# Optimization experiments

Measured on AMD Instinct MI355X. Metric: run time of the kernel, lower is better.

The kernel has to match this reference:

```python
import jax, jax.numpy as jnp
import numpy as np

D_MODEL = 1024
N_HEADS = 16
D_HEAD = D_MODEL // N_HEADS


def setup_inputs() -> dict:
    key = jax.random.key(0)
    ks = jax.random.split(key, 11)
    B, S = 2, 2048
    scale = 1.0 / np.sqrt(D_MODEL)
    inp = {
        "query": jax.random.normal(ks[0], (B, S, D_MODEL), jnp.float32),
        "key": jax.random.normal(ks[1], (B, S, D_MODEL), jnp.float32),
        "value": jax.random.normal(ks[2], (B, S, D_MODEL), jnp.float32),
        "Wq": jax.random.normal(ks[3], (D_MODEL, D_MODEL), jnp.float32) * scale,
        "bq": jnp.zeros((D_MODEL,), jnp.float32),
        "Wk": jax.random.normal(ks[4], (D_MODEL, D_MODEL), jnp.float32) * scale,
        "bk": jnp.zeros((D_MODEL,), jnp.float32),
        "Wv": jax.random.normal(ks[5], (D_MODEL, D_MODEL), jnp.float32) * scale,
        "bv": jnp.zeros((D_MODEL,), jnp.float32),
        "Wo": jax.random.normal(ks[6], (D_MODEL, D_MODEL), jnp.float32) * scale,
        "bo": jnp.zeros((D_MODEL,), jnp.float32),
    }
    return inp


def _split_heads(x):
    B, S, _ = x.shape
    return x.reshape(B, S, N_HEADS, D_HEAD).transpose(0, 2, 1, 3)  # [B,H,S,Dh]


def reference(query, key, value, Wq, bq, Wk, bk, Wv, bv, Wo, bo):
    q = _split_heads(query @ Wq + bq)
    k = _split_heads(key @ Wk + bk)
    v = _split_heads(value @ Wv + bv)
    # scores [B,H,S,S] -- faithfully materialized as in the original
    scores = jnp.einsum("bhqd,bhkd->bhqk", q, k) / np.sqrt(D_HEAD)
    attn = jax.nn.softmax(scores, axis=-1)
    out = jnp.einsum("bhqk,bhkd->bhqd", attn, v)  # [B,H,S,Dh]
    B, H, S, Dh = out.shape
    out = out.transpose(0, 2, 1, 3).reshape(B, S, H * Dh)
    return out @ Wo + bo
```

## Files before the change

kernel.cpp:

```cpp
#include <hip/hip_runtime.h>
#include <hip/hip_bf16.h>

using bf16 = __hip_bfloat16;
typedef __bf16 bf16x8 __attribute__((ext_vector_type(8)));
typedef __bf16 bf16x2v __attribute__((ext_vector_type(2)));
typedef float f32x4 __attribute__((ext_vector_type(4)));
typedef float f32x16 __attribute__((ext_vector_type(16)));

#define SEQ 2048
#define DM  1024
#define QSCALE 0.18033688011112042f

__device__ __forceinline__ f32x4 mfma16(bf16x8 a, bf16x8 b, f32x4 c) {
  return __builtin_amdgcn_mfma_f32_16x16x32_bf16(a, b, c, 0, 0, 0);
}
__device__ __forceinline__ f32x16 mfma32(bf16x8 a, bf16x8 b, f32x16 c) {
  return __builtin_amdgcn_mfma_f32_32x32x16_bf16(a, b, c, 0, 0, 0);
}
__device__ __forceinline__ void gload16(const void* g, void* l) {
  __builtin_amdgcn_global_load_lds(
      (const __attribute__((address_space(1))) unsigned int*)g,
      (__attribute__((address_space(3))) unsigned int*)l, 16, 0, 0);
}
__device__ __forceinline__ unsigned short bfbits(float x) {
  bf16 h = __float2bfloat16(x);
  return *reinterpret_cast<unsigned short*>(&h);
}
__device__ __forceinline__ unsigned pk2(float a, float b) {
#if __has_builtin(__builtin_amdgcn_cvt_pk_bf16_f32)
  bf16x2v r = __builtin_amdgcn_cvt_pk_bf16_f32(a, b);
  return *reinterpret_cast<unsigned*>(&r);
#else
  return (unsigned)bfbits(a) | ((unsigned)bfbits(b) << 16);
#endif
}
__device__ __forceinline__ float fexp2(float x) {
#if __has_builtin(__builtin_amdgcn_exp2f)
  return __builtin_amdgcn_exp2f(x);
#else
  return exp2f(x);
#endif
}
__device__ __forceinline__ void plswap(unsigned& a, unsigned& b) {
  asm("v_permlane32_swap_b32 %0, %1" : "+v"(a), "+v"(b));
}

__global__ __launch_bounds__(256) void cast_all(const float* __restrict__ q,
                                                const float* __restrict__ k,
                                                const float* __restrict__ v,
                                                const float* __restrict__ Wq,
                                                const float* __restrict__ Wk,
                                                const float* __restrict__ Wv,
                                                const float* __restrict__ Wo,
                                                bf16* __restrict__ Lx,
                                                bf16* __restrict__ Lw,
                                                bf16* __restrict__ Lwo) {
  __shared__ float tf[64][68];
  if (blockIdx.y < 3) {
    const float* src = blockIdx.y == 0 ? q : (blockIdx.y == 1 ? k : v);
    bf16* dst = Lx + (size_t)blockIdx.y * (4096ull * 1024) + (size_t)blockIdx.x * 16384;
#pragma unroll
    for (int i = 0; i < 8; ++i) {
      int u = threadIdx.x + i * 256;
      int k32 = u >> 6, l = u & 63;
      const float* p = src + (size_t)(blockIdx.x * 16 + (l & 15)) * 1024 + k32 * 32 + (l >> 4) * 8;
      float4 a = *(const float4*)p;
      float4 b = *(const float4*)(p + 4);
      alignas(16) unsigned o[4] = {pk2(a.x, a.y), pk2(a.z, a.w), pk2(b.x, b.y), pk2(b.z, b.w)};
      *(uint4*)(dst + (size_t)u * 8) = *(const uint4*)o;
    }
    return;
  }
  const int widx = blockIdx.y - 3;
  const float* W = widx == 0 ? Wq : (widx == 1 ? Wk : (widx == 2 ? Wv : Wo));
  bf16* dst = widx < 3 ? (Lw + (size_t)widx * 1048576) : Lwo;
  const int t = threadIdx.x, bx = blockIdx.x & 15, by = blockIdx.x >> 4;
#pragma unroll
  for (int i = 0; i < 4; ++i) {
    int u = t + i * 256, r = u >> 4, c4 = u & 15;
    *(float4*)&tf[r][c4 * 4] = *(const float4*)(W + (size_t)(by * 64 + r) * 1024 + bx * 64 + c4 * 4);
  }
  __syncthreads();
#pragma unroll
  for (int i = 0; i < 2; ++i) {
    int u = t + i * 256;
    int sub = u >> 6, l = u & 63;
    int n16l = sub >> 1, k32l = sub & 1;
    int nn = n16l * 16 + (l & 15);
    int kk = k32l * 32 + (l >> 4) * 8;
    alignas(16) unsigned o[4];
#pragma unroll
    for (int p = 0; p < 4; ++p) o[p] = pk2(tf[kk + 2 * p][nn], tf[kk + 2 * p + 1][nn]);
    size_t off = ((((size_t)(bx * 4 + n16l)) * 32 + (by * 2 + k32l)) * 64 + l) * 8;
    *(uint4*)(dst + off) = *(const uint4*)o;
  }
}

__global__ __launch_bounds__(512, 4) void qkv_gemm(const bf16* __restrict__ Lw,
                                                   const bf16* __restrict__ Lx,
                                                   const float* __restrict__ bq,
                                                   const float* __restrict__ bk,
                                                   const float* __restrict__ bv,
                                                   bf16* __restrict__ Lq,
                                                   bf16* __restrict__ Lk,
                                                   bf16* __restrict__ Lv) {
  __shared__ alignas(16) bf16 At[2][8192];
  __shared__ alignas(16) bf16 Bt[2][4096];
  const int t = threadIdx.x, lane = t & 63, w = t >> 6;
  const int m16 = lane & 15, g4 = lane >> 4;
  const int bid = blockIdx.x;
  const int logical = (bid & 7) * 48 + (bid >> 3);
  const int third = logical >> 7;
  const int r = logical & 127;
  const int shift = third < 2 ? 5 : 3;
  const int mt = r >> shift, nt = r & ((1 << shift) - 1);
  const int wm = w >> 1, wn = w & 1;
  const bf16* Wb = Lw + (size_t)third * 1048576;
  const bf16* Xb = Lx + (size_t)third * (4096ull * 1024);
  const bf16* Asrc = third < 2 ? Wb : Xb;
  const bf16* Bsrc = third < 2 ? Xb : Wb;
  f32x4 acc[4][4] = {};

#pragma unroll
  for (int ii = 0; ii < 3; ++ii) {
    int u = w * 3 + ii;
    if (u < 16)
      gload16(Asrc + (((size_t)(mt * 16 + u) * 32 + 0) * 64 + lane) * 8, (void*)&At[0][u * 512]);
    else
      gload16(Bsrc + (((size_t)(nt * 8 + u - 16) * 32 + 0) * 64 + lane) * 8, (void*)&Bt[0][(u - 16) * 512]);
  }

  int cur = 0;
  for (int k = 0; k < 32; ++k) {
    __builtin_amdgcn_s_barrier();
    __builtin_amdgcn_sched_barrier(0);
    if (k < 31) {
      const int nb = cur ^ 1;
#pragma unroll
      for (int ii = 0; ii < 3; ++ii) {
        int u = w * 3 + ii;
        if (u < 16)
          gload16(Asrc + (((size_t)(mt * 16 + u) * 32 + k + 1) * 64 + lane) * 8, (void*)&At[nb][u * 512]);
        else
          gload16(Bsrc + (((size_t)(nt * 8 + u - 16) * 32 + k + 1) * 64 + lane) * 8,
                  (void*)&Bt[nb][(u - 16) * 512]);
      }
      asm volatile("s_waitcnt vmcnt(3)" ::: "memory");
    } else {
      asm volatile("s_waitcnt vmcnt(0)" ::: "memory");
    }
    __builtin_amdgcn_sched_barrier(0);
    __builtin_amdgcn_s_barrier();
    __builtin_amdgcn_sched_barrier(0);

    bf16x8 afr[4], bfr[4];
#pragma unroll
    for (int i = 0; i < 4; ++i) afr[i] = *(const bf16x8*)&At[cur][(wm * 4 + i) * 512 + lane * 8];
#pragma unroll
    for (int j = 0; j < 4; ++j) bfr[j] = *(const bf16x8*)&Bt[cur][(wn * 4 + j) * 512 + lane * 8];
    __builtin_amdgcn_s_setprio(1);
#pragma unroll
    for (int i = 0; i < 4; ++i)
#pragma unroll
      for (int j = 0; j < 4; ++j) acc[i][j] = mfma16(afr[i], bfr[j], acc[i][j]);
    __builtin_amdgcn_s_setprio(0);
    cur ^= 1;
  }

  if (third < 2) {
    bf16* dst = third == 0 ? Lq : Lk;
    const float* bias = third == 0 ? bq : bk;
    const float sc = third == 0 ? QSCALE : 1.0f;
#pragma unroll
    for (int mi = 0; mi < 4; ++mi) {
      int doutb = mt * 256 + wm * 64 + mi * 16 + g4 * 4;
      float4 b4 = *(const float4*)(bias + doutb);
      int hh = doutb >> 6, d32 = (doutb & 63) >> 5;
      int lhi = (doutb & 31) >> 3, half = g4 & 1;
#pragma unroll
      for (int nj = 0; nj < 4; ++nj) {
        int seq = nt * 128 + wn * 64 + nj * 16 + m16;
        int bb2 = seq >> 11, s16w = (seq & 2047) >> 4;
        size_t off = ((((size_t)(bb2 * 128 + s16w)) * 16 + hh) * 2 + d32) * 512 + (m16 + 16 * lhi) * 8 + half * 4;
        uint2 pv;
        pv.x = pk2((acc[mi][nj][0] + b4.x) * sc, (acc[mi][nj][1] + b4.y) * sc);
        pv.y = pk2((acc[mi][nj][2] + b4.z) * sc, (acc[mi][nj][3] + b4.w) * sc);
        *(uint2*)(dst + off) = pv;
      }
    }
  } else {
#pragma unroll
    for (int nj = 0; nj < 4; ++nj) {
      int dout = nt * 128 + wn * 64 + nj * 16 + m16;
      float bvv = bv[dout];
      int hh = dout >> 6, dt = (dout & 63) >> 4;
#pragma unroll
      for (int mi = 0; mi < 4; ++mi) {
        int seqb = mt * 256 + wm * 64 + mi * 16 + g4 * 4;
        int b_ = seqb >> 11, kt = (seqb & 2047) >> 6, ks32 = (seqb & 63) >> 5;
        int lhi = (seqb & 31) >> 3, half = g4 & 1;
        size_t off = (((((size_t)(b_ * 32 + kt)) * 16 + hh) * 4 + dt) * 2 + ks32) * 512 + (m16 + 16 * lhi) * 8 + half * 4;
        uint2 pv;
        pv.x = pk2(acc[mi][nj][0] + bvv, acc[mi][nj][1] + bvv);
        pv.y = pk2(acc[mi][nj][2] + bvv, acc[mi][nj][3] + bvv);
        *(uint2*)(Lv + off) = pv;
      }
    }
  }
}

__global__ __launch_bounds__(512, 4) void flash(const bf16* __restrict__ Lq,
                                                const bf16* __restrict__ Lk,
                                                const bf16* __restrict__ Lv,
                                                bf16* __restrict__ Lab) {
  __shared__ alignas(16) unsigned char smem[65536];
  bf16* const Kb = (bf16*)smem;
  bf16* const Vb = (bf16*)(smem + 32768);

  const int t = threadIdx.x, lane = t & 63, w = t >> 6;
  const int l31 = lane & 31, m16 = lane & 15, hi = lane >> 5, b4 = (lane >> 4) & 1;
  const int qw = w >> 1, g = w & 1, wg = w >> 1;
  const int bid = blockIdx.x;
  const int logical = ((bid & 7) << 6) | (bid >> 3);
  const int qt = logical & 15, h = (logical >> 4) & 15, b = logical >> 8;

  bf16x8 qf[4];
  {
    const int sQ = b * 128 + qt * 8 + qw * 2 + b4;
#pragma unroll
    for (int ks = 0; ks < 4; ++ks) {
      const int d32 = ks >> 1, g4q = (ks & 1) * 2 + hi;
      qf[ks] = *(const bf16x8*)(Lq + (((size_t)sQ * 16 + h) * 2 + d32) * 512 + (m16 + 16 * g4q) * 8);
    }
  }

  const int ss = wg >> 1, sd = wg & 1;
#pragma unroll
  for (int u = 0; u < 2; ++u) {
    const bf16* gk = Lk + ((((size_t)(b * 128 + g * 64 + u * 2 + ss)) * 16 + h) * 2 + sd) * 512 + lane * 8;
    gload16(gk, (void*)(Kb + (g * 2 + 0) * 4096 + u * 2048 + wg * 512));
    const bf16* gv = Lv + (((((size_t)(b * 32 + g * 16)) * 16 + h) * 4 + wg) * 2 + u) * 512 + lane * 8;
    gload16(gv, (void*)(Vb + (g * 2 + 0) * 4096 + u * 2048 + wg * 512));
  }

  float lrow = 0.f;
  f32x16 oacc[2] = {};
  __syncthreads();

  for (int it = 0; it < 16; ++it) {
    const int cur = it & 1;
    const bf16* const Klb = Kb + (g * 2 + cur) * 4096;
    const bf16* const Vlb = Vb + (g * 2 + cur) * 4096;
    if (it < 15) {
      const int nb = cur ^ 1;
#pragma unroll
      for (int u = 0; u < 2; ++u) {
        const int kc = (it + 1) * 2 + u;
        const bf16* gk = Lk + ((((size_t)(b * 128 + g * 64 + kc * 2 + ss)) * 16 + h) * 2 + sd) * 512 + lane * 8;
        gload16(gk, (void*)(Kb + (g * 2 + nb) * 4096 + u * 2048 + wg * 512));
        const bf16* gv = Lv + (((((size_t)(b * 32 + g * 16 + (kc >> 1))) * 16 + h) * 4 + wg) * 2 + (kc & 1)) * 512 + lane * 8;
        gload16(gv, (void*)(Vb + (g * 2 + nb) * 4096 + u * 2048 + wg * 512));
      }
    }

#pragma unroll
    for (int u = 0; u < 2; ++u) {
      const bf16* const Kl = Klb + u * 2048;
      const bf16* const Vl = Vlb + u * 2048;

      f32x16 s = {};
      __builtin_amdgcn_s_setprio(1);
#pragma unroll
      for (int ks = 0; ks < 4; ++ks) {
        const int d32 = ks >> 1, g4k = (ks & 1) * 2 + hi;
        bf16x8 kf = *(const bf16x8*)&Kl[((b4 * 2 + d32) * 64 + m16 + 16 * g4k) * 8];
        s = mfma32(kf, qf[ks], s);
      }
      __builtin_amdgcn_s_setprio(0);

      float e[16];
#pragma unroll
      for (int r = 0; r < 16; ++r) e[r] = fexp2(s[r]);
      {
        float a0 = e[0] + e[1], a1 = e[2] + e[3], a2 = e[4] + e[5], a3 = e[6] + e[7];
        float a4 = e[8] + e[9], a5 = e[10] + e[11], a6 = e[12] + e[13], a7 = e[14] + e[15];
        lrow += ((a0 + a1) + (a2 + a3)) + ((a4 + a5) + (a6 + a7));
      }
      bf16x8 bP[2];
#pragma unroll
      for (int c = 0; c < 2; ++c) {
        unsigned P0 = pk2(e[8 * c + 0], e[8 * c + 1]);
        unsigned P1 = pk2(e[8 * c + 2], e[8 * c + 3]);
        unsigned P2 = pk2(e[8 * c + 4], e[8 * c + 5]);
        unsigned P3 = pk2(e[8 * c + 6], e[8 * c + 7]);
        plswap(P0, P2);
        plswap(P1, P3);
        alignas(16) unsigned pw[4] = {P0, P1, P2, P3};
        bP[c] = *(const bf16x8*)pw;
      }

      __builtin_amdgcn_s_setprio(1);
#pragma unroll
      for (int dtile = 0; dtile < 2; ++dtile) {
        const int dt = dtile * 2 + b4;
#pragma unroll
        for (int c = 0; c < 2; ++c) {
          bf16x8 av = *(const bf16x8*)&Vl[(dt * 64 + m16 + 16 * (2 * c + hi)) * 8];
          oacc[dtile] = mfma32(av, bP[c], oacc[dtile]);
        }
      }
      __builtin_amdgcn_s_setprio(0);
    }
    __syncthreads();
  }

  lrow += __shfl_xor(lrow, 32);

  float* const Os = (float*)smem;
  float* const Ls = (float*)(smem + 32768);
  if (g == 1) {
#pragma unroll
    for (int dtile = 0; dtile < 2; ++dtile)
#pragma unroll
      for (int r = 0; r < 16; ++r)
        Os[((qw * 2 + dtile) * 16 + r) * 64 + lane] = oacc[dtile][r];
    if (hi == 0) Ls[qw * 32 + l31] = lrow;
  }
  __syncthreads();
  if (g == 0) {
    const float inv = 1.f / (lrow + Ls[qw * 32 + l31]);
    const int sQ = b * 128 + qt * 8 + qw * 2 + b4;
#pragma unroll
    for (int dtile = 0; dtile < 2; ++dtile) {
      const int k32 = h * 2 + dtile;
#pragma unroll
      for (int j = 0; j < 8; ++j) {
        const int r = 2 * j;
        float o0 = oacc[dtile][r] + Os[((qw * 2 + dtile) * 16 + r) * 64 + lane];
        float o1 = oacc[dtile][r + 1] + Os[((qw * 2 + dtile) * 16 + r + 1) * 64 + lane];
        unsigned pv = pk2(o0 * inv, o1 * inv);
        size_t off = ((size_t)sQ * 32 + k32) * 512 + (m16 + 16 * (r >> 2)) * 8 + 4 * hi + (r & 3);
        *(unsigned*)(Lab + off) = pv;
      }
    }
  }
}

__global__ __launch_bounds__(256) void out_gemm(const bf16* __restrict__ Lab,
                                                const bf16* __restrict__ Lwo,
                                                const float* __restrict__ bo,
                                                float* __restrict__ out) {
  __shared__ alignas(16) bf16 Al[2][8192];
  __shared__ alignas(16) bf16 Bl[2][4096];
  const int t = threadIdx.x, lane = t & 63, w = t >> 6;
  const int m16 = lane & 15, g4 = lane >> 4;
  const int bid = blockIdx.y * 16 + blockIdx.x;
  const int logical = (bid & 7) * 64 + (bid >> 3);
  const int nt = logical & 15, mt = logical >> 4;
  const int wm = w >> 1, wn = w & 1;
  f32x4 acc[4][2] = {};

#pragma unroll
  for (int ii = 0; ii < 4; ++ii) {
    int s = w * 4 + ii;
    gload16(Lab + (((size_t)(mt * 8 + (s >> 1))) * 32 + (s & 1)) * 512 + lane * 8, (void*)&Al[0][s * 512]);
  }
#pragma unroll
  for (int ii = 0; ii < 2; ++ii) {
    int s = w * 2 + ii;
    gload16(Lwo + (((size_t)(nt * 4 + (s >> 1))) * 32 + (s & 1)) * 512 + lane * 8, (void*)&Bl[0][s * 512]);
  }

  int cur = 0;
  for (int slab = 0; slab < 16; ++slab) {
    __builtin_amdgcn_s_barrier();
    __builtin_amdgcn_sched_barrier(0);
    if (slab < 15) {
      const int nb = cur ^ 1, ns = slab + 1;
#pragma unroll
      for (int ii = 0; ii < 4; ++ii) {
        int s = w * 4 + ii;
        gload16(Lab + (((size_t)(mt * 8 + (s >> 1))) * 32 + ns * 2 + (s & 1)) * 512 + lane * 8,
                (void*)&Al[nb][s * 512]);
      }
#pragma unroll
      for (int ii = 0; ii < 2; ++ii) {
        int s = w * 2 + ii;
        gload16(Lwo + (((size_t)(nt * 4 + (s >> 1))) * 32 + ns * 2 + (s & 1)) * 512 + lane * 8,
                (void*)&Bl[nb][s * 512]);
      }
      asm volatile("s_waitcnt vmcnt(6)" ::: "memory");
    } else {
      asm volatile("s_waitcnt vmcnt(0)" ::: "memory");
    }
    __builtin_amdgcn_sched_barrier(0);
    __builtin_amdgcn_s_barrier();
    __builtin_amdgcn_sched_barrier(0);
#pragma unroll
    for (int c = 0; c < 2; ++c) {
      bf16x8 aA[4], bW[2];
#pragma unroll
      for (int i = 0; i < 4; ++i) aA[i] = *(const bf16x8*)&Al[cur][((wm * 4 + i) * 2 + c) * 512 + lane * 8];
#pragma unroll
      for (int j = 0; j < 2; ++j) bW[j] = *(const bf16x8*)&Bl[cur][((wn * 2 + j) * 2 + c) * 512 + lane * 8];
      __builtin_amdgcn_s_setprio(1);
#pragma unroll
      for (int i = 0; i < 4; ++i)
#pragma unroll
        for (int j = 0; j < 2; ++j) acc[i][j] = mfma16(aA[i], bW[j], acc[i][j]);
      __builtin_amdgcn_s_setprio(0);
    }
    cur ^= 1;
  }
#pragma unroll
  for (int j = 0; j < 2; ++j) {
    int n = nt * 64 + wn * 32 + j * 16 + m16;
    float bb = bo[n];
#pragma unroll
    for (int i = 0; i < 4; ++i) {
      int seqb = mt * 128 + wm * 64 + i * 16 + g4 * 4;
#pragma unroll
      for (int r = 0; r < 4; ++r) out[(size_t)(seqb + r) * 1024 + n] = acc[i][j][r] + bb;
    }
  }
}

extern "C" void kernel_launch(void* const* d_in, const int* in_sizes, int n_in,
                              void* d_out, int out_size, void* d_ws, size_t ws_size,
                              hipStream_t stream) {
  const float* query = (const float*)d_in[0];
  const float* key   = (const float*)d_in[1];
  const float* value = (const float*)d_in[2];
  const float* Wq = (const float*)d_in[3];
  const float* bq = (const float*)d_in[4];
  const float* Wk = (const float*)d_in[5];
  const float* bk = (const float*)d_in[6];
  const float* Wv = (const float*)d_in[7];
  const float* bv = (const float*)d_in[8];
  const float* Wo = (const float*)d_in[9];
  const float* bo = (const float*)d_in[10];
  float* out = (float*)d_out;

  bf16* Lw  = (bf16*)d_ws;
  bf16* Lwo = Lw + 3ull * 1048576;
  bf16* Lx  = Lwo + 1048576;
  bf16* Lq  = Lx + 3ull * 4194304;
  bf16* Lk  = Lq + 4194304;
  bf16* Lv  = Lk + 4194304;
  bf16* Lab = Lv + 4194304;

  cast_all<<<dim3(256, 7), 256, 0, stream>>>(query, key, value, Wq, Wk, Wv, Wo, Lx, Lw, Lwo);
  qkv_gemm<<<384, 512, 0, stream>>>(Lw, Lx, bq, bk, bv, Lq, Lk, Lv);
  flash<<<512, 512, 0, stream>>>(Lq, Lk, Lv, Lab);
  out_gemm<<<dim3(16, 32), 256, 0, stream>>>(Lab, Lwo, bo, out);
}
```

Before: 210.4 us.

## Split flash attention over two key halves and add combine kernel

Each flash block now covers half of the key sequence, which doubles the grid to 1024 blocks, halves the shared-memory tile buffers and raises the launch-bounds occupancy hint. Each block writes unnormalised fp32 partial outputs and row sums, and a new combine kernel adds the two halves, normalises and packs to bf16. The aim is more parallelism and occupancy in the attention stage. In exchange it adds a kernel launch and extra fp32 global traffic for the partials, reusing the output and input-cast buffers as scratch.

```diff
diff --git a/kernel.cpp b/kernel.cpp
--- a/kernel.cpp
+++ b/kernel.cpp
@@ -209,38 +209,39 @@
   }
 }
 
-__global__ __launch_bounds__(512, 4) void flash(const bf16* __restrict__ Lq,
+__global__ __launch_bounds__(512, 8) void flash(const bf16* __restrict__ Lq,
                                                 const bf16* __restrict__ Lk,
                                                 const bf16* __restrict__ Lv,
-                                                bf16* __restrict__ Lab) {
-  __shared__ alignas(16) unsigned char smem[65536];
+                                                float* __restrict__ Op0,
+                                                float* __restrict__ Op1,
+                                                float* __restrict__ lpart) {
+  __shared__ alignas(16) unsigned char smem[33280];
   bf16* const Kb = (bf16*)smem;
-  bf16* const Vb = (bf16*)(smem + 32768);
+  bf16* const Vb = (bf16*)(smem + 16384);
 
   const int t = threadIdx.x, lane = t & 63, w = t >> 6;
   const int l31 = lane & 31, m16 = lane & 15, hi = lane >> 5, b4 = (lane >> 4) & 1;
   const int qw = w >> 1, g = w & 1, wg = w >> 1;
   const int bid = blockIdx.x;
-  const int logical = ((bid & 7) << 6) | (bid >> 3);
-  const int qt = logical & 15, h = (logical >> 4) & 15, b = logical >> 8;
-
+  const int logical = ((bid & 7) << 7) | (bid >> 3);
+  const int kh = logical & 1, qt = (logical >> 1) & 15, h = (logical >> 5) & 15, b = logical >> 9;
+
+  const int sQ = b * 128 + qt * 8 + qw * 2 + b4;
   bf16x8 qf[4];
+#pragma unroll
+  for (int ks = 0; ks < 4; ++ks) {
+    const int d32 = ks >> 1, g4q = (ks & 1) * 2 + hi;
+    qf[ks] = *(const bf16x8*)(Lq + (((size_t)sQ * 16 + h) * 2 + d32) * 512 + (m16 + 16 * g4q) * 8);
+  }
+
+  const int ss = wg >> 1, sd = wg & 1;
+  const int s16base = b * 128 + kh * 64 + g * 32;
+  const int ktbase = kh * 16 + g * 8;
   {
-    const int sQ = b * 128 + qt * 8 + qw * 2 + b4;
-#pragma unroll
-    for (int ks = 0; ks < 4; ++ks) {
-      const int d32 = ks >> 1, g4q = (ks & 1) * 2 + hi;
-      qf[ks] = *(const bf16x8*)(Lq + (((size_t)sQ * 16 + h) * 2 + d32) * 512 + (m16 + 16 * g4q) * 8);
-    }
-  }
-
-  const int ss = wg >> 1, sd = wg & 1;
-#pragma unroll
-  for (int u = 0; u < 2; ++u) {
-    const bf16* gk = Lk + ((((size_t)(b * 128 + g * 64 + u * 2 + ss)) * 16 + h) * 2 + sd) * 512 + lane * 8;
-    gload16(gk, (void*)(Kb + (g * 2 + 0) * 4096 + u * 2048 + wg * 512));
-    const bf16* gv = Lv + (((((size_t)(b * 32 + g * 16)) * 16 + h) * 4 + wg) * 2 + u) * 512 + lane * 8;
-    gload16(gv, (void*)(Vb + (g * 2 + 0) * 4096 + u * 2048 + wg * 512));
+    const bf16* gk = Lk + ((((size_t)(s16base + ss)) * 16 + h) * 2 + sd) * 512 + lane * 8;
+    gload16(gk, (void*)(Kb + (g * 2 + 0) * 2048 + wg * 512));
+    const bf16* gv = Lv + (((((size_t)(b * 32 + ktbase)) * 16 + h) * 4 + wg) * 2 + 0) * 512 + lane * 8;
+    gload16(gv, (void*)(Vb + (g * 2 + 0) * 2048 + wg * 512));
   }
 
   float lrow = 0.f;
@@ -249,68 +250,58 @@
 
   for (int it = 0; it < 16; ++it) {
     const int cur = it & 1;
-    const bf16* const Klb = Kb + (g * 2 + cur) * 4096;
-    const bf16* const Vlb = Vb + (g * 2 + cur) * 4096;
+    const bf16* const Kl = Kb + (g * 2 + cur) * 2048;
+    const bf16* const Vl = Vb + (g * 2 + cur) * 2048;
     if (it < 15) {
-      const int nb = cur ^ 1;
-#pragma unroll
-      for (int u = 0; u < 2; ++u) {
-        const int kc = (it + 1) * 2 + u;
-        const bf16* gk = Lk + ((((size_t)(b * 128 + g * 64 + kc * 2 + ss)) * 16 + h) * 2 + sd) * 512 + lane * 8;
-        gload16(gk, (void*)(Kb + (g * 2 + nb) * 4096 + u * 2048 + wg * 512));
-        const bf16* gv = Lv + (((((size_t)(b * 32 + g * 16 + (kc >> 1))) * 16 + h) * 4 + wg) * 2 + (kc & 1)) * 512 + lane * 8;
-        gload16(gv, (void*)(Vb + (g * 2 + nb) * 4096 + u * 2048 + wg * 512));
-      }
-    }
-
-#pragma unroll
-    for (int u = 0; u < 2; ++u) {
-      const bf16* const Kl = Klb + u * 2048;
-      const bf16* const Vl = Vlb + u * 2048;
-
-      f32x16 s = {};
-      __builtin_amdgcn_s_setprio(1);
-#pragma unroll
-      for (int ks = 0; ks < 4; ++ks) {
-        const int d32 = ks >> 1, g4k = (ks & 1) * 2 + hi;
-        bf16x8 kf = *(const bf16x8*)&Kl[((b4 * 2 + d32) * 64 + m16 + 16 * g4k) * 8];
-        s = mfma32(kf, qf[ks], s);
-      }
-      __builtin_amdgcn_s_setprio(0);
-
-      float e[16];
-#pragma unroll
-      for (int r = 0; r < 16; ++r) e[r] = fexp2(s[r]);
-      {
-        float a0 = e[0] + e[1], a1 = e[2] + e[3], a2 = e[4] + e[5], a3 = e[6] + e[7];
-        float a4 = e[8] + e[9], a5 = e[10] + e[11], a6 = e[12] + e[13], a7 = e[14] + e[15];
-        lrow += ((a0 + a1) + (a2 + a3)) + ((a4 + a5) + (a6 + a7));
-      }
-      bf16x8 bP[2];
+      const int nb = cur ^ 1, kc = it + 1;
+      const bf16* gk = Lk + ((((size_t)(s16base + kc * 2 + ss)) * 16 + h) * 2 + sd) * 512 + lane * 8;
+      gload16(gk, (void*)(Kb + (g * 2 + nb) * 2048 + wg * 512));
+      const bf16* gv = Lv + (((((size_t)(b * 32 + ktbase + (kc >> 1))) * 16 + h) * 4 + wg) * 2 + (kc & 1)) * 512 + lane * 8;
+      gload16(gv, (void*)(Vb + (g * 2 + nb) * 2048 + wg * 512));
+    }
+
+    f32x16 s = {};
+    __builtin_amdgcn_s_setprio(1);
+#pragma unroll
+    for (int ks = 0; ks < 4; ++ks) {
+      const int d32 = ks >> 1, g4k = (ks & 1) * 2 + hi;
+      bf16x8 kf = *(const bf16x8*)&Kl[((b4 * 2 + d32) * 64 + m16 + 16 * g4k) * 8];
+      s = mfma32(kf, qf[ks], s);
+    }
+    __builtin_amdgcn_s_setprio(0);
+
+    float e[16];
+#pragma unroll
+    for (int r = 0; r < 16; ++r) e[r] = fexp2(s[r]);
+    {
+      float a0 = e[0] + e[1], a1 = e[2] + e[3], a2 = e[4] + e[5], a3 = e[6] + e[7];
+      float a4 = e[8] + e[9], a5 = e[10] + e[11], a6 = e[12] + e[13], a7 = e[14] + e[15];
+      lrow += ((a0 + a1) + (a2 + a3)) + ((a4 + a5) + (a6 + a7));
+    }
+    bf16x8 bP[2];
+#pragma unroll
+    for (int c = 0; c < 2; ++c) {
+      unsigned P0 = pk2(e[8 * c + 0], e[8 * c + 1]);
+      unsigned P1 = pk2(e[8 * c + 2], e[8 * c + 3]);
+      unsigned P2 = pk2(e[8 * c + 4], e[8 * c + 5]);
+      unsigned P3 = pk2(e[8 * c + 6], e[8 * c + 7]);
+      plswap(P0, P2);
+      plswap(P1, P3);
+      alignas(16) unsigned pw[4] = {P0, P1, P2, P3};
+      bP[c] = *(const bf16x8*)pw;
+    }
+
+    __builtin_amdgcn_s_setprio(1);
+#pragma unroll
+    for (int dtile = 0; dtile < 2; ++dtile) {
+      const int dt = dtile * 2 + b4;
 #pragma unroll
       for (int c = 0; c < 2; ++c) {
-        unsigned P0 = pk2(e[8 * c + 0], e[8 * c + 1]);
-        unsigned P1 = pk2(e[8 * c + 2], e[8 * c + 3]);
-        unsigned P2 = pk2(e[8 * c + 4], e[8 * c + 5]);
-        unsigned P3 = pk2(e[8 * c + 6], e[8 * c + 7]);
-        plswap(P0, P2);
-        plswap(P1, P3);
-        alignas(16) unsigned pw[4] = {P0, P1, P2, P3};
-        bP[c] = *(const bf16x8*)pw;
-      }
-
-      __builtin_amdgcn_s_setprio(1);
-#pragma unroll
-      for (int dtile = 0; dtile < 2; ++dtile) {
-        const int dt = dtile * 2 + b4;
-#pragma unroll
-        for (int c = 0; c < 2; ++c) {
-          bf16x8 av = *(const bf16x8*)&Vl[(dt * 64 + m16 + 16 * (2 * c + hi)) * 8];
-          oacc[dtile] = mfma32(av, bP[c], oacc[dtile]);
-        }
-      }
-      __builtin_amdgcn_s_setprio(0);
-    }
+        bf16x8 av = *(const bf16x8*)&Vl[(dt * 64 + m16 + 16 * (2 * c + hi)) * 8];
+        oacc[dtile] = mfma32(av, bP[c], oacc[dtile]);
+      }
+    }
+    __builtin_amdgcn_s_setprio(0);
     __syncthreads();
   }
 
@@ -328,8 +319,9 @@
   }
   __syncthreads();
   if (g == 0) {
-    const float inv = 1.f / (lrow + Ls[qw * 32 + l31]);
-    const int sQ = b * 128 + qt * 8 + qw * 2 + b4;
+    const float lsum = lrow + Ls[qw * 32 + l31];
+    float* const Op = kh ? Op1 : Op0;
+    if (hi == 0) lpart[(((kh * 4096) + sQ * 16 + m16) << 4) + h] = lsum;
 #pragma unroll
     for (int dtile = 0; dtile < 2; ++dtile) {
       const int k32 = h * 2 + dtile;
@@ -338,12 +330,32 @@
         const int r = 2 * j;
         float o0 = oacc[dtile][r] + Os[((qw * 2 + dtile) * 16 + r) * 64 + lane];
         float o1 = oacc[dtile][r + 1] + Os[((qw * 2 + dtile) * 16 + r + 1) * 64 + lane];
-        unsigned pv = pk2(o0 * inv, o1 * inv);
         size_t off = ((size_t)sQ * 32 + k32) * 512 + (m16 + 16 * (r >> 2)) * 8 + 4 * hi + (r & 3);
-        *(unsigned*)(Lab + off) = pv;
-      }
-    }
-  }
+        float2 pv;
+        pv.x = o0;
+        pv.y = o1;
+        *(float2*)(Op + off) = pv;
+      }
+    }
+  }
+}
+
+__global__ __launch_bounds__(256) void combine(const float* __restrict__ Op0,
+                                               const float* __restrict__ Op1,
+                                               const float* __restrict__ lpart,
+                                               bf16* __restrict__ Lab) {
+  const int s = blockIdx.x * 256 + threadIdx.x;
+  const size_t off = (size_t)s * 2;
+  const int w8 = (int)(off & 511);
+  const int sQ = (int)(off >> 14);
+  const int k32 = (int)((off >> 9) & 31);
+  const int h = k32 >> 1;
+  const int m16 = (w8 >> 3) & 15;
+  const int q = sQ * 16 + m16;
+  const float inv = 1.f / (lpart[(q << 4) + h] + lpart[((4096 + q) << 4) + h]);
+  float2 a = *(const float2*)(Op0 + off);
+  float2 b = *(const float2*)(Op1 + off);
+  *(unsigned*)(Lab + off) = pk2((a.x + b.x) * inv, (a.y + b.y) * inv);
 }
 
 __global__ __launch_bounds__(256) void out_gemm(const bf16* __restrict__ Lab,
@@ -449,8 +461,13 @@
   bf16* Lv  = Lk + 4194304;
   bf16* Lab = Lv + 4194304;
 
+  float* Op0   = out;
+  float* Op1   = (float*)Lx;
+  float* lpart = (float*)Lx + 4194304;
+
   cast_all<<<dim3(256, 7), 256, 0, stream>>>(query, key, value, Wq, Wk, Wv, Wo, Lx, Lw, Lwo);
   qkv_gemm<<<384, 512, 0, stream>>>(Lw, Lx, bq, bk, bv, Lq, Lk, Lv);
-  flash<<<512, 512, 0, stream>>>(Lq, Lk, Lv, Lab);
+  flash<<<1024, 512, 0, stream>>>(Lq, Lk, Lv, Op0, Op1, lpart);
+  combine<<<8192, 256, 0, stream>>>(Op0, Op1, lpart, Lab);
   out_gemm<<<dim3(16, 32), 256, 0, stream>>>(Lab, Lwo, bo, out);
 }
```

Result: slower. 333.0 us (+58.3%).

## Triple-buffer QKV GEMM loads and compute softmax row sums via MFMA

Applied to the files above, without the earlier changes.

The QKV projection GEMM moves from double to triple buffering in LDS, prefetching two k-steps ahead with adjusted vmcnt waits so more global-load latency is hidden. In the flash kernel, the per-lane scalar summation of exponentials (plus a cross-lane shuffle) is replaced by two extra MFMAs against an all-ones bf16 operand that accumulate row sums in the matrix unit. This trades VALU adds for MFMA work but rounds the sums from bf16 P values and adds 16 accumulator registers. Triple buffering raises LDS use per block, which may limit occupancy at four blocks per CU.

```diff
diff --git a/kernel.cpp b/kernel.cpp
--- a/kernel.cpp
+++ b/kernel.cpp
@@ -104,8 +104,8 @@
                                                    bf16* __restrict__ Lq,
                                                    bf16* __restrict__ Lk,
                                                    bf16* __restrict__ Lv) {
-  __shared__ alignas(16) bf16 At[2][8192];
-  __shared__ alignas(16) bf16 Bt[2][4096];
+  __shared__ alignas(16) bf16 At[3][8192];
+  __shared__ alignas(16) bf16 Bt[3][4096];
   const int t = threadIdx.x, lane = t & 63, w = t >> 6;
   const int m16 = lane & 15, g4 = lane >> 4;
   const int bid = blockIdx.x;
@@ -122,29 +122,34 @@
   f32x4 acc[4][4] = {};
 
 #pragma unroll
-  for (int ii = 0; ii < 3; ++ii) {
-    int u = w * 3 + ii;
-    if (u < 16)
-      gload16(Asrc + (((size_t)(mt * 16 + u) * 32 + 0) * 64 + lane) * 8, (void*)&At[0][u * 512]);
-    else
-      gload16(Bsrc + (((size_t)(nt * 8 + u - 16) * 32 + 0) * 64 + lane) * 8, (void*)&Bt[0][(u - 16) * 512]);
-  }
-
-  int cur = 0;
+  for (int s0 = 0; s0 < 2; ++s0) {
+#pragma unroll
+    for (int ii = 0; ii < 3; ++ii) {
+      int u = w * 3 + ii;
+      if (u < 16)
+        gload16(Asrc + (((size_t)(mt * 16 + u) * 32 + s0) * 64 + lane) * 8, (void*)&At[s0][u * 512]);
+      else
+        gload16(Bsrc + (((size_t)(nt * 8 + u - 16) * 32 + s0) * 64 + lane) * 8, (void*)&Bt[s0][(u - 16) * 512]);
+    }
+  }
+
   for (int k = 0; k < 32; ++k) {
+    const int cb = k % 3;
     __builtin_amdgcn_s_barrier();
     __builtin_amdgcn_sched_barrier(0);
-    if (k < 31) {
-      const int nb = cur ^ 1;
+    if (k < 30) {
+      const int nb = (k + 2) % 3;
 #pragma unroll
       for (int ii = 0; ii < 3; ++ii) {
         int u = w * 3 + ii;
         if (u < 16)
-          gload16(Asrc + (((size_t)(mt * 16 + u) * 32 + k + 1) * 64 + lane) * 8, (void*)&At[nb][u * 512]);
+          gload16(Asrc + (((size_t)(mt * 16 + u) * 32 + k + 2) * 64 + lane) * 8, (void*)&At[nb][u * 512]);
         else
-          gload16(Bsrc + (((size_t)(nt * 8 + u - 16) * 32 + k + 1) * 64 + lane) * 8,
+          gload16(Bsrc + (((size_t)(nt * 8 + u - 16) * 32 + k + 2) * 64 + lane) * 8,
                   (void*)&Bt[nb][(u - 16) * 512]);
       }
+      asm volatile("s_waitcnt vmcnt(6)" ::: "memory");
+    } else if (k == 30) {
       asm volatile("s_waitcnt vmcnt(3)" ::: "memory");
     } else {
       asm volatile("s_waitcnt vmcnt(0)" ::: "memory");
@@ -155,16 +160,15 @@
 
     bf16x8 afr[4], bfr[4];
 #pragma unroll
-    for (int i = 0; i < 4; ++i) afr[i] = *(const bf16x8*)&At[cur][(wm * 4 + i) * 512 + lane * 8];
-#pragma unroll
-    for (int j = 0; j < 4; ++j) bfr[j] = *(const bf16x8*)&Bt[cur][(wn * 4 + j) * 512 + lane * 8];
+    for (int i = 0; i < 4; ++i) afr[i] = *(const bf16x8*)&At[cb][(wm * 4 + i) * 512 + lane * 8];
+#pragma unroll
+    for (int j = 0; j < 4; ++j) bfr[j] = *(const bf16x8*)&Bt[cb][(wn * 4 + j) * 512 + lane * 8];
     __builtin_amdgcn_s_setprio(1);
 #pragma unroll
     for (int i = 0; i < 4; ++i)
 #pragma unroll
       for (int j = 0; j < 4; ++j) acc[i][j] = mfma16(afr[i], bfr[j], acc[i][j]);
     __builtin_amdgcn_s_setprio(0);
-    cur ^= 1;
   }
 
   if (third < 2) {
@@ -224,6 +228,9 @@
   const int logical = ((bid & 7) << 6) | (bid >> 3);
   const int qt = logical & 15, h = (logical >> 4) & 15, b = logical >> 8;
 
+  alignas(16) const unsigned onesw[4] = {0x3F803F80u, 0x3F803F80u, 0x3F803F80u, 0x3F803F80u};
+  const bf16x8 onesf = *(const bf16x8*)onesw;
+
   bf16x8 qf[4];
   {
     const int sQ = b * 128 + qt * 8 + qw * 2 + b4;
@@ -243,7 +250,7 @@
     gload16(gv, (void*)(Vb + (g * 2 + 0) * 4096 + u * 2048 + wg * 512));
   }
 
-  float lrow = 0.f;
+  f32x16 lacc = {};
   f32x16 oacc[2] = {};
   __syncthreads();
 
@@ -281,11 +288,6 @@
       float e[16];
 #pragma unroll
       for (int r = 0; r < 16; ++r) e[r] = fexp2(s[r]);
-      {
-        float a0 = e[0] + e[1], a1 = e[2] + e[3], a2 = e[4] + e[5], a3 = e[6] + e[7];
-        float a4 = e[8] + e[9], a5 = e[10] + e[11], a6 = e[12] + e[13], a7 = e[14] + e[15];
-        lrow += ((a0 + a1) + (a2 + a3)) + ((a4 + a5) + (a6 + a7));
-      }
       bf16x8 bP[2];
 #pragma unroll
       for (int c = 0; c < 2; ++c) {
@@ -309,12 +311,14 @@
           oacc[dtile] = mfma32(av, bP[c], oacc[dtile]);
         }
       }
+      lacc = mfma32(onesf, bP[0], lacc);
+      lacc = mfma32(onesf, bP[1], lacc);
       __builtin_amdgcn_s_setprio(0);
     }
     __syncthreads();
   }
 
-  lrow += __shfl_xor(lrow, 32);
+  const float lv = lacc[0];
 
   float* const Os = (float*)smem;
   float* const Ls = (float*)(smem + 32768);
@@ -324,11 +328,11 @@
 #pragma unroll
       for (int r = 0; r < 16; ++r)
         Os[((qw * 2 + dtile) * 16 + r) * 64 + lane] = oacc[dtile][r];
-    if (hi == 0) Ls[qw * 32 + l31] = lrow;
+    if (hi == 0) Ls[qw * 32 + l31] = lv;
   }
   __syncthreads();
   if (g == 0) {
-    const float inv = 1.f / (lrow + Ls[qw * 32 + l31]);
+    const float inv = 1.f / (lv + Ls[qw * 32 + l31]);
     const int sQ = b * 128 + qt * 8 + qw * 2 + b4;
 #pragma unroll
     for (int dtile = 0; dtile < 2; ++dtile) {
```

Result: no change. 211.0 us (+0.3%).
